# Kernel tuning notes

Measured on AMD Instinct MI355X. Metric: run time of the kernel, lower is better.

## Reference

```python
import jax, jax.numpy as jnp
import numpy as np

N_SPLIT = 4096   # split tokens (coarse octree levels)
N_VQ    = 12288  # VQ tokens (finest level)
N       = N_SPLIT + N_VQ
C       = 256    # num_embed
H       = 8      # num_heads
L       = 4      # num_blocks
P       = 256    # patch_size (attention window)
DIL     = 2      # dilation for odd (swin) blocks
DVQ     = 32     # vqvae embedding_channels
VQ_SIZE = 256    # vqvae embedding_sizes
VQ_G    = 4      # vqvae quantizer_group
HID     = 4 * C


def _layernorm(x, s, b):
    m = x.mean(-1, keepdims=True)
    v = jnp.var(x, axis=-1, keepdims=True)
    return (x - m) * jax.lax.rsqrt(v + 1e-5) * s + b


def _sin_pos_emb(n, c):
    pos = jnp.arange(n, dtype=jnp.float32)[:, None]
    half = c // 2
    freqs = jnp.exp(-jnp.log(10000.0) * jnp.arange(half, dtype=jnp.float32) / half)
    ang = pos * freqs
    return jnp.concatenate([jnp.sin(ang), jnp.cos(ang)], axis=-1)


def _forward(split, zq, targets_vq, category, batch_id, mask, d2b,
             split_emb, class_emb, vq_proj_w, vq_proj_b,
             ln1_s, ln1_b, qkv_w, qkv_b, attn_w, attn_b,
             ln2_s, ln2_b, fc1_w, fc1_b, fc2_w, fc2_b,
             lnx_s, lnx_b, split_w, split_b, vq_w, vq_b):
    # token embeddings: [split tokens ; projected VQ codes]
    x = jnp.concatenate([split_emb[split], zq @ vq_proj_w + vq_proj_b], axis=0)  # [N,C]
    cond = class_emb[category]                      # [B,C]
    x = jnp.where(mask[:, None], cond[batch_id], x)  # masked tokens -> class cond

    # depth2batch gather, then OctFormer blocks
    xb = x[d2b] + _sin_pos_emb(N, C).astype(x.dtype)
    dh = C // H
    scale = dh ** -0.5
    for l in range(L):
        d = DIL if (l % 2 == 1) else 1  # swin-style alternating dilation
        h = _layernorm(xb, ln1_s[l], ln1_b[l])
        # dilated window partition: window j in a super-window holds tokens base+p*d+j
        hw = h.reshape(-1, P, d, C).transpose(0, 2, 1, 3).reshape(-1, P, C)
        qkv = hw @ qkv_w[l] + qkv_b[l]              # [nw,P,3C]
        q, k, v = [t.reshape(-1, P, H, dh) for t in jnp.split(qkv, 3, axis=-1)]
        att = jax.nn.softmax(jnp.einsum('wphd,wqhd->whpq', q, k) * scale, axis=-1)
        o = jnp.einsum('whpq,wqhd->wphd', att, v).reshape(-1, P, C) @ attn_w[l] + attn_b[l]
        o = o.reshape(-1, d, P, C).transpose(0, 2, 1, 3).reshape(-1, C)  # undo partition
        xb = xb + o
        h = _layernorm(xb, ln2_s[l], ln2_b[l])
        xb = xb + (jax.nn.gelu(h @ fc1_w[l] + fc1_b[l]) @ fc2_w[l] + fc2_b[l])
    # batch2depth scatter (inverse permutation)
    x = jnp.zeros_like(xb).at[d2b].set(xb)
    x = _layernorm(x, lnx_s, lnx_b)

    # split head + masked cross-entropy
    sl = x[:N_SPLIT] @ split_w + split_b            # [Ns,2]
    ms = mask[:N_SPLIT].astype(jnp.float32)
    ce_s = -jnp.take_along_axis(jax.nn.log_softmax(sl, axis=-1), split[:, None], axis=-1)[:, 0]
    split_loss = jnp.sum(ce_s * ms) / jnp.maximum(jnp.sum(ms), 1.0)

    # vq head + masked grouped cross-entropy
    vl = (x[N_SPLIT:] @ vq_w + vq_b).reshape(N_VQ, VQ_G, VQ_SIZE)
    mv = mask[N_SPLIT:].astype(jnp.float32)
    ce_v = -jnp.take_along_axis(jax.nn.log_softmax(vl, axis=-1), targets_vq[..., None], axis=-1)[..., 0]
    vq_loss = jnp.sum(ce_v.mean(-1) * mv) / jnp.maximum(jnp.sum(mv), 1.0)
    return jnp.stack([split_loss, vq_loss])


def setup_inputs() -> dict:
    key = jax.random.key(0)
    ks = jax.random.split(key, 16)
    s = 0.02
    inp = {
        'split': jax.random.randint(ks[0], (N_SPLIT,), 0, 2),
        'zq': jax.random.normal(ks[1], (N_VQ, DVQ), jnp.float32),
        'targets_vq': jax.random.randint(ks[2], (N_VQ, VQ_G), 0, VQ_SIZE),
        'category': jnp.zeros((1,), jnp.int32),
        'batch_id': jnp.zeros((N,), jnp.int32),
        'mask': jax.random.randint(ks[3], (N,), 0, 2).astype(bool),
        'd2b': jax.random.permutation(ks[4], N),
        'split_emb': s * jax.random.normal(ks[5], (2, C), jnp.float32),
        'class_emb': s * jax.random.normal(ks[6], (1, C), jnp.float32),
        'vq_proj_w': s * jax.random.normal(ks[7], (DVQ, C), jnp.float32),
        'vq_proj_b': jnp.zeros((C,), jnp.float32),
        'ln1_s': jnp.ones((L, C), jnp.float32),
        'ln1_b': jnp.zeros((L, C), jnp.float32),
        'qkv_w': s * jax.random.normal(ks[8], (L, C, 3 * C), jnp.float32),
        'qkv_b': jnp.zeros((L, 3 * C), jnp.float32),
        'attn_w': s * jax.random.normal(ks[9], (L, C, C), jnp.float32),
        'attn_b': jnp.zeros((L, C), jnp.float32),
        'ln2_s': jnp.ones((L, C), jnp.float32),
        'ln2_b': jnp.zeros((L, C), jnp.float32),
        'fc1_w': s * jax.random.normal(ks[10], (L, C, HID), jnp.float32),
        'fc1_b': jnp.zeros((L, HID), jnp.float32),
        'fc2_w': s * jax.random.normal(ks[11], (L, HID, C), jnp.float32),
        'fc2_b': jnp.zeros((L, C), jnp.float32),
        'lnx_s': jnp.ones((C,), jnp.float32),
        'lnx_b': jnp.zeros((C,), jnp.float32),
        'split_w': s * jax.random.normal(ks[12], (C, 2), jnp.float32),
        'split_b': jnp.zeros((2,), jnp.float32),
        'vq_w': s * jax.random.normal(ks[13], (C, VQ_G * VQ_SIZE), jnp.float32),
        'vq_b': jnp.zeros((VQ_G * VQ_SIZE,), jnp.float32),
    }
    return inp


def reference(split, zq, targets_vq, category, batch_id, mask, d2b,
              split_emb, class_emb, vq_proj_w, vq_proj_b,
              ln1_s, ln1_b, qkv_w, qkv_b, attn_w, attn_b,
              ln2_s, ln2_b, fc1_w, fc1_b, fc2_w, fc2_b,
              lnx_s, lnx_b, split_w, split_b, vq_w, vq_b):
    return _forward(split, zq, targets_vq, category, batch_id, mask, d2b,
                    split_emb, class_emb, vq_proj_w, vq_proj_b,
                    ln1_s, ln1_b, qkv_w, qkv_b, attn_w, attn_b,
                    ln2_s, ln2_b, fc1_w, fc1_b, fc2_w, fc2_b,
                    lnx_s, lnx_b, split_w, split_b, vq_w, vq_b)
```

## Files before the change

kernel.cpp:

```cpp
#include <hip/hip_runtime.h>
#include <hip/hip_bf16.h>
#include <math.h>

#define NSPLIT 4096
#define NVQ    12288
#define NTOK   16384
#define CH     256
#define NH     8
#define DHD    32
#define NL     4
#define PW     256
#define HIDN   1024
#define DVQ    32
#define VQG    4
#define VQS    256

typedef __attribute__((ext_vector_type(8))) short bf16x8;
typedef __attribute__((ext_vector_type(4))) float f32x4;

typedef const __attribute__((address_space(1))) void* gas_ptr;
typedef __attribute__((address_space(3))) void* las_ptr;
#define GLD16(g, s) __builtin_amdgcn_global_load_lds((gas_ptr)(g), (las_ptr)(s), 16, 0, 0)

static __device__ __forceinline__ unsigned pack2bf(float a, float b) {
    __hip_bfloat16 ha = __float2bfloat16(a), hb = __float2bfloat16(b);
    return ((unsigned)*(unsigned short*)&hb << 16) | *(unsigned short*)&ha;
}
static __device__ __forceinline__ float bf2f(unsigned short s) {
    unsigned u = (unsigned)s << 16;
    return *(float*)&u;
}
static __device__ __forceinline__ unsigned short f2bfu(float f) {
    __hip_bfloat16 h = __float2bfloat16(f);
    return *(unsigned short*)&h;
}

__global__ void k_wt_all(const float* __restrict__ qkv_w, const float* __restrict__ attn_w,
                         const float* __restrict__ fc1_w, const float* __restrict__ fc2_w,
                         const float* __restrict__ vq_w,
                         short* __restrict__ qkvT, short* __restrict__ attnT,
                         short* __restrict__ fc1T, short* __restrict__ fc2T,
                         short* __restrict__ vqT,
                         const void* __restrict__ mask_raw, int* __restrict__ mode) {
    int b = blockIdx.x;
    if (b == 832) {
        __shared__ int c_even, c_odd, c_0100;
        const unsigned short* u16 = (const unsigned short*)mask_raw;
        if (threadIdx.x == 0) { c_even = 0; c_odd = 0; c_0100 = 0; }
        __syncthreads();
        int le = 0, lo = 0, l01 = 0;
        for (int i = threadIdx.x; i < 8192; i += 256) {
            unsigned short v = u16[i];
            if (v == 0x3F80u) { if (i & 1) lo++; else le++; }
            if (v == 0x0100u) l01++;
        }
        atomicAdd(&c_even, le); atomicAdd(&c_odd, lo); atomicAdd(&c_0100, l01);
        __syncthreads();
        if (threadIdx.x == 0) {
            int m;
            if      (c_even > 500) m = 2;
            else if (c_odd  > 500) m = 3;
            else if (c_0100 > 500) m = 1;
            else                   m = 0;
            *mode = m;
        }
        return;
    }
    const float* W; short* Wt; int K, N, tn, tk;
    if (b < 192)      { int r = b;       int z = r / 48; r %= 48; K = 256;  N = 768;
                        tk = r / 12; tn = r % 12;
                        W = qkv_w + (size_t)z * K * N; Wt = qkvT + (size_t)z * K * N; }
    else if (b < 256) { int r = b - 192; int z = r / 16; r %= 16; K = 256;  N = 256;
                        tk = r / 4;  tn = r % 4;
                        W = attn_w + (size_t)z * K * N; Wt = attnT + (size_t)z * K * N; }
    else if (b < 512) { int r = b - 256; int z = r / 64; r %= 64; K = 256;  N = 1024;
                        tk = r / 16; tn = r % 16;
                        W = fc1_w + (size_t)z * K * N; Wt = fc1T + (size_t)z * K * N; }
    else if (b < 768) { int r = b - 512; int z = r / 64; r %= 64; K = 1024; N = 256;
                        tk = r / 4;  tn = r % 4;
                        W = fc2_w + (size_t)z * K * N; Wt = fc2T + (size_t)z * K * N; }
    else              { int r = b - 768; K = 256; N = 1024;
                        tk = r / 16; tn = r % 16; W = vq_w; Wt = vqT; }
    __shared__ float t[64][65];
    int bn = tn * 64, bk = tk * 64, tid = threadIdx.x;
#pragma unroll
    for (int it = 0; it < 16; ++it) {
        int idx = it * 256 + tid; int r = idx >> 6, c = idx & 63;
        t[r][c] = W[(size_t)(bk + r) * N + bn + c];
    }
    __syncthreads();
#pragma unroll
    for (int it = 0; it < 16; ++it) {
        int idx = it * 256 + tid; int r = idx >> 6, c = idx & 63;
        __hip_bfloat16 h = __float2bfloat16(t[c][r]);
        Wt[(size_t)(bn + r) * K + bk + c] = *(short*)&h;
    }
}

__global__ void k_embed_gather(const int* __restrict__ split, const float* __restrict__ zq,
                               const int* __restrict__ category, const int* __restrict__ batch_id,
                               const void* __restrict__ mask_raw, const int* __restrict__ mode,
                               int* __restrict__ mask_i, const int* __restrict__ d2b,
                               const float* __restrict__ split_emb, const float* __restrict__ class_emb,
                               const float* __restrict__ vq_proj_w, const float* __restrict__ vq_proj_b,
                               const float* __restrict__ ln1s, const float* __restrict__ ln1b,
                               unsigned short* __restrict__ xbv, unsigned short* __restrict__ hb) {
    int j = blockIdx.x, c = threadIdx.x;
    int i = d2b[j];
    int m = *mode, mv;
    if      (m == 0) mv = ((const int*)mask_raw)[i] != 0;
    else if (m == 1) mv = ((const unsigned char*)mask_raw)[i] != 0;
    else if (m == 2) mv = ((const unsigned short*)mask_raw)[i] != 0;
    else             mv = ((const unsigned int*)mask_raw)[i] != 0;
    if (c == 0) mask_i[i] = mv;
    float v;
    if (mv) {
        v = class_emb[category[batch_id[i]] * CH + c];
    } else if (i < NSPLIT) {
        v = split_emb[split[i] * CH + c];
    } else {
        const float* z = zq + (size_t)(i - NSPLIT) * DVQ;
        float acc = vq_proj_b[c];
#pragma unroll
        for (int k = 0; k < DVQ; k++) acc += z[k] * vq_proj_w[k * CH + c];
        v = acc;
    }
    const float kneg = -0.07195578415606394f;
    float jf = (float)j, pe;
    if (c < 128) { float f = expf(c * kneg);         pe = sinf(jf * f); }
    else         { float f = expf((c - 128) * kneg); pe = cosf(jf * f); }
    v += pe;
    float s = v, sq = v * v;
#pragma unroll
    for (int o = 32; o; o >>= 1) { s += __shfl_xor(s, o); sq += __shfl_xor(sq, o); }
    __shared__ float ps[4], pq[4];
    if ((c & 63) == 0) { ps[c >> 6] = s; pq[c >> 6] = sq; }
    __syncthreads();
    float S = ps[0] + ps[1] + ps[2] + ps[3];
    float Q = pq[0] + pq[1] + pq[2] + pq[3];
    float mean = S * (1.0f / CH);
    float var  = Q * (1.0f / CH) - mean * mean;
    float rsf = rsqrtf(var + 1e-5f);
    xbv[(size_t)j * CH + c] = f2bfu(v);
    hb[(size_t)j * CH + c]  = f2bfu((v - mean) * rsf * ln1s[c] + ln1b[c]);
}

template <int GELU>
__global__ __launch_bounds__(256, 4) void k_mm(
    const short* __restrict__ A, const short* __restrict__ Bt,
    const float* __restrict__ bias, unsigned short* __restrict__ outB,
    int N, int K) {
    __shared__ short As[2][128 * 32];
    __shared__ short Bs[2][128 * 32];
    const int tid = threadIdx.x;
    const int w = tid >> 6, l = tid & 63;
    const int bm = blockIdx.y * 128, bn = blockIdx.x * 128;
    const int wr = w >> 1, wc = w & 1;
    const int q = l >> 4, rA = l & 15;
    const int srow = w * 16 + (l >> 2);
    const int sx = ((l & 3) ^ ((l >> 2) & 3)) * 8;
    const int fx = (q ^ (rA & 3)) * 8;

    const short* gA0 = A + (size_t)(bm + srow) * K + sx;
    const short* gA1 = A + (size_t)(bm + srow + 64) * K + sx;
    const short* gB0 = Bt + (size_t)(bn + srow) * K + sx;
    const short* gB1 = Bt + (size_t)(bn + srow + 64) * K + sx;
    short* lA0 = &As[0][w * 16 * 32];
    short* lA1 = &As[0][(64 + w * 16) * 32];
    short* lA0h = &As[1][w * 16 * 32];
    short* lA1h = &As[1][(64 + w * 16) * 32];
    short* lB0 = &Bs[0][w * 16 * 32];
    short* lB1 = &Bs[0][(64 + w * 16) * 32];
    short* lB0h = &Bs[1][w * 16 * 32];
    short* lB1h = &Bs[1][(64 + w * 16) * 32];

    f32x4 acc[4][4] = {};

    for (int k0 = 0; k0 < K; k0 += 64) {
        GLD16(gA0 + k0, lA0);       GLD16(gA1 + k0, lA1);
        GLD16(gA0 + k0 + 32, lA0h); GLD16(gA1 + k0 + 32, lA1h);
        GLD16(gB0 + k0, lB0);       GLD16(gB1 + k0, lB1);
        GLD16(gB0 + k0 + 32, lB0h); GLD16(gB1 + k0 + 32, lB1h);
        __syncthreads();
#pragma unroll
        for (int s = 0; s < 2; s++) {
            bf16x8 a[4], b[4];
#pragma unroll
            for (int m = 0; m < 4; m++)
                a[m] = *(const bf16x8*)(&As[s][(wr * 64 + m * 16 + rA) * 32 + fx]);
#pragma unroll
            for (int n = 0; n < 4; n++)
                b[n] = *(const bf16x8*)(&Bs[s][(wc * 64 + n * 16 + rA) * 32 + fx]);
#pragma unroll
            for (int m = 0; m < 4; m++)
#pragma unroll
                for (int n = 0; n < 4; n++)
                    acc[m][n] = __builtin_amdgcn_mfma_f32_16x16x32_bf16(b[n], a[m], acc[m][n], 0, 0, 0);
        }
        __syncthreads();
    }

#pragma unroll
    for (int m = 0; m < 4; m++) {
        int row = bm + wr * 64 + m * 16 + rA;
#pragma unroll
        for (int n = 0; n < 4; n++) {
            int colb = bn + wc * 64 + n * 16 + q * 4;
            float4 bv = *(const float4*)(bias + colb);
            float v0 = acc[m][n][0] + bv.x;
            float v1 = acc[m][n][1] + bv.y;
            float v2 = acc[m][n][2] + bv.z;
            float v3 = acc[m][n][3] + bv.w;
            if (GELU) {
                float t0 = tanhf(0.7978845608028654f * (v0 + 0.044715f * v0 * v0 * v0));
                float t1 = tanhf(0.7978845608028654f * (v1 + 0.044715f * v1 * v1 * v1));
                float t2 = tanhf(0.7978845608028654f * (v2 + 0.044715f * v2 * v2 * v2));
                float t3 = tanhf(0.7978845608028654f * (v3 + 0.044715f * v3 * v3 * v3));
                v0 = 0.5f * v0 * (1.0f + t0); v1 = 0.5f * v1 * (1.0f + t1);
                v2 = 0.5f * v2 * (1.0f + t2); v3 = 0.5f * v3 * (1.0f + t3);
            }
            ushort4 st = { f2bfu(v0), f2bfu(v1), f2bfu(v2), f2bfu(v3) };
            *(ushort4*)(outB + (size_t)row * N + colb) = st;
        }
    }
}

template <int LNOUT>
__global__ __launch_bounds__(512, 4) void k_mm_row(
    const short* __restrict__ A, const short* __restrict__ Bt,
    const float* __restrict__ bias, unsigned short* __restrict__ xbv,
    const float* __restrict__ lns, const float* __restrict__ lnb,
    unsigned short* __restrict__ h_out, const int* __restrict__ d2b, int K,
    const int* __restrict__ split, const int* __restrict__ mask_i,
    const float* __restrict__ sw, const float* __restrict__ sb,
    float* __restrict__ sce) {
    __shared__ short As[2][32 * 32];
    __shared__ short Bs[2][256 * 32];
    __shared__ float part[2][8][32];
    const int tid = threadIdx.x;
    const int w = tid >> 6, l = tid & 63;
    const int bm = blockIdx.x * 32;
    const int q = l >> 4, rA = l & 15;
    const int sx = ((l & 3) ^ ((l >> 2) & 3)) * 8;
    const int fx = (q ^ (rA & 3)) * 8;

    const short* gA = A + (size_t)(bm + (l >> 2)) * K + sx;
    const short* gB = Bt + (size_t)(w * 32 + (l >> 2)) * K + sx;

    f32x4 acc[2][2] = {};

    for (int k0 = 0; k0 < K; k0 += 64) {
        if (w == 0) {
#pragma unroll
            for (int rg = 0; rg < 2; rg++) {
                GLD16(gA + (size_t)(rg * 16) * K + k0,      &As[0][(rg * 16) * 32]);
                GLD16(gA + (size_t)(rg * 16) * K + k0 + 32, &As[1][(rg * 16) * 32]);
            }
        }
#pragma unroll
        for (int i = 0; i < 2; i++) {
            GLD16(gB + (size_t)(i * 16) * K + k0,      &Bs[0][(w * 32 + i * 16) * 32]);
            GLD16(gB + (size_t)(i * 16) * K + k0 + 32, &Bs[1][(w * 32 + i * 16) * 32]);
        }
        __syncthreads();
#pragma unroll
        for (int s = 0; s < 2; s++) {
            bf16x8 a[2], b[2];
#pragma unroll
            for (int m = 0; m < 2; m++)
                a[m] = *(const bf16x8*)(&As[s][(m * 16 + rA) * 32 + fx]);
#pragma unroll
            for (int n = 0; n < 2; n++)
                b[n] = *(const bf16x8*)(&Bs[s][(w * 32 + n * 16 + rA) * 32 + fx]);
#pragma unroll
            for (int m = 0; m < 2; m++)
#pragma unroll
                for (int n = 0; n < 2; n++)
                    acc[m][n] = __builtin_amdgcn_mfma_f32_16x16x32_bf16(b[n], a[m], acc[m][n], 0, 0, 0);
        }
        __syncthreads();
    }

    float rsum[2] = {}, rsq[2] = {};
#pragma unroll
    for (int m = 0; m < 2; m++) {
        int row = bm + m * 16 + rA;
#pragma unroll
        for (int n = 0; n < 2; n++) {
            int colb = w * 32 + n * 16 + q * 4;
            float4 bv = *(const float4*)(bias + colb);
            size_t oi = (size_t)row * CH + colb;
            ushort4 xo = *(const ushort4*)(xbv + oi);
            float v0 = acc[m][n][0] + bv.x + bf2f(xo.x);
            float v1 = acc[m][n][1] + bv.y + bf2f(xo.y);
            float v2 = acc[m][n][2] + bv.z + bf2f(xo.z);
            float v3 = acc[m][n][3] + bv.w + bf2f(xo.w);
            acc[m][n][0] = v0; acc[m][n][1] = v1; acc[m][n][2] = v2; acc[m][n][3] = v3;
            if (LNOUT != 2) {
                ushort4 st = { f2bfu(v0), f2bfu(v1), f2bfu(v2), f2bfu(v3) };
                *(ushort4*)(xbv + oi) = st;
            }
            rsum[m] += (v0 + v1) + (v2 + v3);
            rsq[m]  += (v0 * v0 + v1 * v1) + (v2 * v2 + v3 * v3);
        }
    }
    if (LNOUT) {
#pragma unroll
        for (int m = 0; m < 2; m++) {
            rsum[m] += __shfl_xor(rsum[m], 16); rsum[m] += __shfl_xor(rsum[m], 32);
            rsq[m]  += __shfl_xor(rsq[m], 16);  rsq[m]  += __shfl_xor(rsq[m], 32);
        }
        if (q == 0) {
#pragma unroll
            for (int m = 0; m < 2; m++) {
                part[0][w][m * 16 + rA] = rsum[m];
                part[1][w][m * 16 + rA] = rsq[m];
            }
        }
        __syncthreads();
#pragma unroll
        for (int m = 0; m < 2; m++) {
            int row = m * 16 + rA;
            float S = 0.f, Q = 0.f;
#pragma unroll
            for (int ww = 0; ww < 8; ww++) { S += part[0][ww][row]; Q += part[1][ww][row]; }
            float mean = S * (1.0f / CH);
            float var  = Q * (1.0f / CH) - mean * mean;
            float rsf = rsqrtf(var + 1e-5f);
            size_t orow = (LNOUT == 2) ? (size_t)d2b[bm + row] : (size_t)(bm + row);
#pragma unroll
            for (int n = 0; n < 2; n++) {
                int colb = w * 32 + n * 16 + q * 4;
                float4 sv = *(const float4*)(lns + colb);
                float4 bb = *(const float4*)(lnb + colb);
                float h0 = (acc[m][n][0] - mean) * rsf * sv.x + bb.x;
                float h1 = (acc[m][n][1] - mean) * rsf * sv.y + bb.y;
                float h2 = (acc[m][n][2] - mean) * rsf * sv.z + bb.z;
                float h3 = (acc[m][n][3] - mean) * rsf * sv.w + bb.w;
                acc[m][n][0] = h0; acc[m][n][1] = h1; acc[m][n][2] = h2; acc[m][n][3] = h3;
                ushort4 st = { f2bfu(h0), f2bfu(h1), f2bfu(h2), f2bfu(h3) };
                *(ushort4*)(h_out + orow * CH + colb) = st;
            }
        }
    }
    if (LNOUT == 2) {
        float a0[2] = {}, a1[2] = {};
#pragma unroll
        for (int m = 0; m < 2; m++) {
#pragma unroll
            for (int n = 0; n < 2; n++) {
                int colb = w * 32 + n * 16 + q * 4;
#pragma unroll
                for (int j = 0; j < 4; j++) {
                    a0[m] += acc[m][n][j] * sw[2 * (colb + j)];
                    a1[m] += acc[m][n][j] * sw[2 * (colb + j) + 1];
                }
            }
            a0[m] += __shfl_xor(a0[m], 16); a0[m] += __shfl_xor(a0[m], 32);
            a1[m] += __shfl_xor(a1[m], 16); a1[m] += __shfl_xor(a1[m], 32);
        }
        __syncthreads();
        if (q == 0) {
#pragma unroll
            for (int m = 0; m < 2; m++) {
                part[0][w][m * 16 + rA] = a0[m];
                part[1][w][m * 16 + rA] = a1[m];
            }
        }
        __syncthreads();
        if (w == 0 && q == 0) {
#pragma unroll
            for (int m = 0; m < 2; m++) {
                int row = m * 16 + rA;
                int orow = d2b[bm + row];
                if (orow < NSPLIT) {
                    float l0 = sb[0], l1 = sb[1];
#pragma unroll
                    for (int ww = 0; ww < 8; ww++) { l0 += part[0][ww][row]; l1 += part[1][ww][row]; }
                    float mx = fmaxf(l0, l1);
                    float lse = mx + logf(__expf(l0 - mx) + __expf(l1 - mx));
                    float ce = lse - (split[orow] ? l1 : l0);
                    sce[orow] = ce * (float)mask_i[orow];
                }
            }
        }
    }
}

__global__ __launch_bounds__(256, 4) void k_vq_head(
    const short* __restrict__ A, const short* __restrict__ vqT,
    const float* __restrict__ vq_b, const int* __restrict__ targets,
    float* __restrict__ vce4) {
    __shared__ short As[2][32 * 32];
    __shared__ short Bs[2][256 * 32];
    __shared__ float part[2][4][32];
    __shared__ float tgtv[32];
    const int tid = threadIdx.x;
    const int w = tid >> 6, l = tid & 63;
    const int bm = blockIdx.x * 32;
    const int g = blockIdx.y;
    const int q = l >> 4, rA = l & 15;
    const int sx = ((l & 3) ^ ((l >> 2) & 3)) * 8;
    const int fx = (q ^ (rA & 3)) * 8;

    const short* gA = A + (size_t)(bm + (l >> 2)) * CH + sx;
    const short* gB = vqT + (size_t)(g * VQS + w * 64 + (l >> 2)) * CH + sx;

    f32x4 acc[2][4] = {};

    for (int k0 = 0; k0 < CH; k0 += 64) {
        if (w == 0) {
#pragma unroll
            for (int rg = 0; rg < 2; rg++) {
                GLD16(gA + (size_t)(rg * 16) * CH + k0,      &As[0][(rg * 16) * 32]);
                GLD16(gA + (size_t)(rg * 16) * CH + k0 + 32, &As[1][(rg * 16) * 32]);
            }
        }
#pragma unroll
        for (int i = 0; i < 4; i++) {
            GLD16(gB + (size_t)(i * 16) * CH + k0,      &Bs[0][(w * 64 + i * 16) * 32]);
            GLD16(gB + (size_t)(i * 16) * CH + k0 + 32, &Bs[1][(w * 64 + i * 16) * 32]);
        }
        __syncthreads();
#pragma unroll
        for (int s = 0; s < 2; s++) {
            bf16x8 a[2], b[4];
#pragma unroll
            for (int m = 0; m < 2; m++)
                a[m] = *(const bf16x8*)(&As[s][(m * 16 + rA) * 32 + fx]);
#pragma unroll
            for (int n = 0; n < 4; n++)
                b[n] = *(const bf16x8*)(&Bs[s][(w * 64 + n * 16 + rA) * 32 + fx]);
#pragma unroll
            for (int m = 0; m < 2; m++)
#pragma unroll
                for (int n = 0; n < 4; n++)
                    acc[m][n] = __builtin_amdgcn_mfma_f32_16x16x32_bf16(b[n], a[m], acc[m][n], 0, 0, 0);
        }
        __syncthreads();
    }

    float pm[2];
#pragma unroll
    for (int m = 0; m < 2; m++) {
        pm[m] = -1e30f;
        int row = m * 16 + rA;
        int t = targets[(size_t)(bm + row) * VQG + g];
#pragma unroll
        for (int n = 0; n < 4; n++) {
            int colb = w * 64 + n * 16 + q * 4;
            float4 bv = *(const float4*)(vq_b + g * VQS + colb);
            float v0 = acc[m][n][0] + bv.x;
            float v1 = acc[m][n][1] + bv.y;
            float v2 = acc[m][n][2] + bv.z;
            float v3 = acc[m][n][3] + bv.w;
            acc[m][n][0] = v0; acc[m][n][1] = v1; acc[m][n][2] = v2; acc[m][n][3] = v3;
            if (colb + 0 == t) tgtv[row] = v0;
            if (colb + 1 == t) tgtv[row] = v1;
            if (colb + 2 == t) tgtv[row] = v2;
            if (colb + 3 == t) tgtv[row] = v3;
            pm[m] = fmaxf(pm[m], fmaxf(fmaxf(v0, v1), fmaxf(v2, v3)));
        }
    }
#pragma unroll
    for (int m = 0; m < 2; m++) {
        pm[m] = fmaxf(pm[m], __shfl_xor(pm[m], 16));
        pm[m] = fmaxf(pm[m], __shfl_xor(pm[m], 32));
    }
    if (q == 0) {
#pragma unroll
        for (int m = 0; m < 2; m++) part[0][w][m * 16 + rA] = pm[m];
    }
    __syncthreads();
    float pmf[2], psum[2];
#pragma unroll
    for (int m = 0; m < 2; m++) {
        int row = m * 16 + rA;
        float mx = fmaxf(fmaxf(part[0][0][row], part[0][1][row]),
                         fmaxf(part[0][2][row], part[0][3][row]));
        pmf[m] = mx;
        float s = 0.f;
#pragma unroll
        for (int n = 0; n < 4; n++)
            s += __expf(acc[m][n][0] - mx) + __expf(acc[m][n][1] - mx)
               + __expf(acc[m][n][2] - mx) + __expf(acc[m][n][3] - mx);
        psum[m] = s;
    }
#pragma unroll
    for (int m = 0; m < 2; m++) {
        psum[m] += __shfl_xor(psum[m], 16);
        psum[m] += __shfl_xor(psum[m], 32);
    }
    if (q == 0) {
#pragma unroll
        for (int m = 0; m < 2; m++) part[1][w][m * 16 + rA] = psum[m];
    }
    __syncthreads();
    if (w == 0 && q == 0) {
#pragma unroll
        for (int m = 0; m < 2; m++) {
            int row = m * 16 + rA;
            float tot = part[1][0][row] + part[1][1][row] + part[1][2][row] + part[1][3][row];
            float lse = pmf[m] + logf(tot);
            vce4[(size_t)(bm + row) * VQG + g] = lse - tgtv[row];
        }
    }
}

__global__ __launch_bounds__(512, 4) void k_attn_fused(
    const unsigned short* __restrict__ hin, const short* __restrict__ Wt,
    const float* __restrict__ bias, short* __restrict__ o, int dil) {
    __shared__ short smem[40960];
    short* Asm = smem;
    short* Wsm = smem + 16384;
    short* Ql  = smem;
    short* Kl  = smem + 8192;
    short* Vt  = smem + 16384;
    short* Pl  = smem + 24576;

    const int wid = blockIdx.x, hd = blockIdx.y;
    const int tid = threadIdx.x;
    const int w = tid >> 6, l = tid & 63;
    const int g = l >> 4, c = l & 15;
    const int tbase = (wid / dil) * (PW * dil) + (wid % dil);
    const int sx = ((l & 3) ^ ((l >> 2) & 3)) * 8;
    const int fx = (g ^ (c & 3)) * 8;

    f32x4 acc[2][6] = {};
    {
        const int lr = l >> 2;
        const int rw = w * 12 + lr;
        const int seg = rw >> 5, within = rw & 31;
        const short* gW = Wt + (size_t)(seg * 256 + hd * 32 + within) * CH + sx;
        for (int k0 = 0; k0 < CH; k0 += 64) {
#pragma unroll
            for (int h16 = 0; h16 < 2; h16++) {
                int row = w * 32 + h16 * 16 + lr;
                const unsigned short* src = hin + (size_t)(tbase + row * dil) * CH + k0 + sx;
                GLD16(src,      Asm + (w * 32 + h16 * 16) * 32);
                GLD16(src + 32, Asm + 8192 + (w * 32 + h16 * 16) * 32);
            }
            if (l < 48) {
                GLD16(gW + k0,      Wsm + (w * 12) * 32);
                GLD16(gW + k0 + 32, Wsm + 3072 + (w * 12) * 32);
            }
            __syncthreads();
#pragma unroll
            for (int s = 0; s < 2; s++) {
                bf16x8 a[2], b[6];
#pragma unroll
                for (int m = 0; m < 2; m++)
                    a[m] = *(const bf16x8*)(Asm + s * 8192 + (w * 32 + m * 16 + c) * 32 + fx);
#pragma unroll
                for (int n = 0; n < 6; n++)
                    b[n] = *(const bf16x8*)(Wsm + s * 3072 + (n * 16 + c) * 32 + fx);
#pragma unroll
                for (int m = 0; m < 2; m++)
#pragma unroll
                    for (int n = 0; n < 6; n++)
                        acc[m][n] = __builtin_amdgcn_mfma_f32_16x16x32_bf16(b[n], a[m], acc[m][n], 0, 0, 0);
            }
            __syncthreads();
        }
    }
#pragma unroll
    for (int m = 0; m < 2; m++) {
        int t = w * 32 + m * 16 + c;
#pragma unroll
        for (int n = 0; n < 6; n++) {
            int seg = n >> 1, n1 = n & 1;
            int colb = n1 * 16 + g * 4;
            float4 bv = *(const float4*)(bias + seg * 256 + hd * 32 + colb);
            float v0 = acc[m][n][0] + bv.x;
            float v1 = acc[m][n][1] + bv.y;
            float v2 = acc[m][n][2] + bv.z;
            float v3 = acc[m][n][3] + bv.w;
            if (seg < 2) {
                short* dst = (seg == 0) ? Ql : Kl;
                int slot = (n1 * 2 + (g >> 1)) ^ (t & 3);
                uint2 pk; pk.x = pack2bf(v0, v1); pk.y = pack2bf(v2, v3);
                *(uint2*)(dst + t * 32 + slot * 8 + (g & 1) * 4) = pk;
            } else {
                int d0 = colb;
                Vt[(d0 + 0) * PW + ((((t >> 3) ^ ((d0 + 0) & 7))) << 3) + (t & 7)] = (short)f2bfu(v0);
                Vt[(d0 + 1) * PW + ((((t >> 3) ^ ((d0 + 1) & 7))) << 3) + (t & 7)] = (short)f2bfu(v1);
                Vt[(d0 + 2) * PW + ((((t >> 3) ^ ((d0 + 2) & 7))) << 3) + (t & 7)] = (short)f2bfu(v2);
                Vt[(d0 + 3) * PW + ((((t >> 3) ^ ((d0 + 3) & 7))) << 3) + (t & 7)] = (short)f2bfu(v3);
            }
        }
    }
    __syncthreads();

    bf16x8 qf[2];
#pragma unroll
    for (int qt = 0; qt < 2; qt++) {
        int qrow = w * 32 + qt * 16 + c;
        qf[qt] = *(const bf16x8*)(Ql + qrow * 32 + ((g ^ (qrow & 3)) * 8));
    }

    f32x4 acco[2][2] = {};
    float m_s[2] = {-1e30f, -1e30f};
    float l_s[2] = {0.f, 0.f};
    const float scale = 0.17677669529663687f;

#pragma unroll
    for (int ch = 0; ch < 4; ch++) {
        bf16x8 kf[4];
#pragma unroll
        for (int kvt = 0; kvt < 4; kvt++) {
            int kv = ch * 64 + kvt * 16 + c;
            kf[kvt] = *(const bf16x8*)(Kl + kv * 32 + ((g ^ (kv & 3)) * 8));
        }
        f32x4 accs[4][2] = {};
#pragma unroll
        for (int kvt = 0; kvt < 4; kvt++)
#pragma unroll
            for (int qt = 0; qt < 2; qt++)
                accs[kvt][qt] = __builtin_amdgcn_mfma_f32_16x16x32_bf16(kf[kvt], qf[qt], accs[kvt][qt], 0, 0, 0);

        float fb[2];
#pragma unroll
        for (int qt = 0; qt < 2; qt++) {
            float mx = -1e30f;
#pragma unroll
            for (int kvt = 0; kvt < 4; kvt++) {
                mx = fmaxf(mx, fmaxf(fmaxf(accs[kvt][qt][0], accs[kvt][qt][1]),
                                     fmaxf(accs[kvt][qt][2], accs[kvt][qt][3])));
            }
            mx = fmaxf(mx, __shfl_xor(mx, 16));
            mx = fmaxf(mx, __shfl_xor(mx, 32));
            float mnew = fmaxf(m_s[qt], mx * scale);
            fb[qt] = __expf(m_s[qt] - mnew);
            m_s[qt] = mnew;
        }
#pragma unroll
        for (int mt = 0; mt < 2; mt++) {
            float fo = fb[mt];
#pragma unroll
            for (int r = 0; r < 4; r++) {
                acco[mt][0][r] *= fo;
                acco[mt][1][r] *= fo;
            }
        }
        float rsum[2] = {0.f, 0.f};
#pragma unroll
        for (int kvt = 0; kvt < 4; kvt++) {
            const int cchunk = kvt * 2 + (g >> 1);
            const int koff = (g & 1) << 2;
#pragma unroll
            for (int qt = 0; qt < 2; qt++) {
                float p0 = __expf(accs[kvt][qt][0] * scale - m_s[qt]);
                float p1 = __expf(accs[kvt][qt][1] * scale - m_s[qt]);
                float p2 = __expf(accs[kvt][qt][2] * scale - m_s[qt]);
                float p3 = __expf(accs[kvt][qt][3] * scale - m_s[qt]);
                rsum[qt] += (p0 + p1) + (p2 + p3);
                int qq = qt * 16 + c;
                int phys = cchunk ^ (qq & 7);
                uint2 pk; pk.x = pack2bf(p0, p1); pk.y = pack2bf(p2, p3);
                *(uint2*)(Pl + w * 2048 + qq * 64 + phys * 8 + koff) = pk;
            }
        }
#pragma unroll
        for (int qt = 0; qt < 2; qt++) {
            float s = rsum[qt];
            s += __shfl_xor(s, 16);
            s += __shfl_xor(s, 32);
            l_s[qt] = l_s[qt] * fb[qt] + s;
        }
#pragma unroll
        for (int ks = 0; ks < 2; ks++) {
            bf16x8 pa[2];
#pragma unroll
            for (int mt = 0; mt < 2; mt++) {
                int qq = mt * 16 + c;
                int phys = (ks * 4 + g) ^ (qq & 7);
                pa[mt] = *(const bf16x8*)(Pl + w * 2048 + qq * 64 + phys * 8);
            }
#pragma unroll
            for (int nt = 0; nt < 2; nt++) {
                int d = nt * 16 + c;
                int kvabs = ch * 64 + ks * 32 + g * 8;
                int phys = (kvabs >> 3) ^ (d & 7);
                bf16x8 vb = *(const bf16x8*)(Vt + d * PW + phys * 8);
#pragma unroll
                for (int mt = 0; mt < 2; mt++)
                    acco[mt][nt] = __builtin_amdgcn_mfma_f32_16x16x32_bf16(vb, pa[mt], acco[mt][nt], 0, 0, 0);
            }
        }
    }

#pragma unroll
    for (int mt = 0; mt < 2; mt++) {
        float linv = 1.0f / l_s[mt];
        int qrow = w * 32 + mt * 16 + c;
        size_t trow = (size_t)(tbase + qrow * dil) * CH + hd * DHD;
#pragma unroll
        for (int nt = 0; nt < 2; nt++) {
            ushort4 st = { f2bfu(acco[mt][nt][0] * linv), f2bfu(acco[mt][nt][1] * linv),
                           f2bfu(acco[mt][nt][2] * linv), f2bfu(acco[mt][nt][3] * linv) };
            *(ushort4*)((unsigned short*)o + trow + nt * 16 + g * 4) = st;
        }
    }
}

__global__ void k_reduce(const float* __restrict__ sce, const float* __restrict__ vce4,
                         const int* __restrict__ mask_i, float* __restrict__ out) {
    int tid = threadIdx.x;
    float s1 = 0, s2 = 0, s3 = 0, s4 = 0;
    for (int i = tid; i < NSPLIT; i += 256) { s1 += sce[i]; s2 += (float)mask_i[i]; }
    for (int i = tid; i < NVQ; i += 256) {
        float mv = (float)mask_i[NSPLIT + i];
        float cs = vce4[i * 4 + 0] + vce4[i * 4 + 1] + vce4[i * 4 + 2] + vce4[i * 4 + 3];
        s3 += cs * 0.25f * mv;
        s4 += mv;
    }
    __shared__ float r1[256], r2[256], r3[256], r4[256];
    r1[tid] = s1; r2[tid] = s2; r3[tid] = s3; r4[tid] = s4;
    __syncthreads();
    for (int o = 128; o; o >>= 1) {
        if (tid < o) { r1[tid] += r1[tid + o]; r2[tid] += r2[tid + o];
                       r3[tid] += r3[tid + o]; r4[tid] += r4[tid + o]; }
        __syncthreads();
    }
    if (tid == 0) {
        out[0] = r1[0] / fmaxf(r2[0], 1.0f);
        out[1] = r3[0] / fmaxf(r4[0], 1.0f);
    }
}

extern "C" void kernel_launch(void* const* d_in, const int* in_sizes, int n_in,
                              void* d_out, int out_size, void* d_ws, size_t ws_size,
                              hipStream_t stream) {
    const int*   split      = (const int*)d_in[0];
    const float* zq         = (const float*)d_in[1];
    const int*   targets_vq = (const int*)d_in[2];
    const int*   category   = (const int*)d_in[3];
    const int*   batch_id   = (const int*)d_in[4];
    const void*  mask_raw   = d_in[5];
    const int*   d2b        = (const int*)d_in[6];
    const float* split_emb  = (const float*)d_in[7];
    const float* class_emb  = (const float*)d_in[8];
    const float* vq_proj_w  = (const float*)d_in[9];
    const float* vq_proj_b  = (const float*)d_in[10];
    const float* ln1_s      = (const float*)d_in[11];
    const float* ln1_b      = (const float*)d_in[12];
    const float* qkv_w      = (const float*)d_in[13];
    const float* qkv_b      = (const float*)d_in[14];
    const float* attn_w     = (const float*)d_in[15];
    const float* attn_b     = (const float*)d_in[16];
    const float* ln2_s      = (const float*)d_in[17];
    const float* ln2_b      = (const float*)d_in[18];
    const float* fc1_w      = (const float*)d_in[19];
    const float* fc1_b      = (const float*)d_in[20];
    const float* fc2_w      = (const float*)d_in[21];
    const float* fc2_b      = (const float*)d_in[22];
    const float* lnx_s      = (const float*)d_in[23];
    const float* lnx_b      = (const float*)d_in[24];
    const float* sw         = (const float*)d_in[25];
    const float* sb         = (const float*)d_in[26];
    const float* vq_w       = (const float*)d_in[27];
    const float* vq_b       = (const float*)d_in[28];

    char* ws = (char*)d_ws;
    int* mode   = (int*)ws;
    int* mask_i = (int*)(ws + 256);
    float* sce  = (float*)(ws + 256 + 4 * NTOK);
    float* vce4 = sce + NSPLIT;
    char* p = ws + (1 << 20);
    short* qkvT = (short*)p;  p += (size_t)NL * 768 * CH * 2;
    short* attnT = (short*)p; p += (size_t)NL * CH * CH * 2;
    short* fc1T = (short*)p;  p += (size_t)NL * HIDN * CH * 2;
    short* fc2T = (short*)p;  p += (size_t)NL * CH * HIDN * 2;
    short* vqT = (short*)p;   p += (size_t)HIDN * CH * 2;
    unsigned short* xbv = (unsigned short*)p; p += (size_t)NTOK * CH * 2;
    unsigned short* h_bf = (unsigned short*)p; p += (size_t)NTOK * CH * 2;
    unsigned short* o_bf = (unsigned short*)p; p += (size_t)NTOK * CH * 2;
    short* big = (short*)p;

    k_wt_all<<<833, 256, 0, stream>>>(qkv_w, attn_w, fc1_w, fc2_w, vq_w,
                                      qkvT, attnT, fc1T, fc2T, vqT, mask_raw, mode);
    k_embed_gather<<<NTOK, 256, 0, stream>>>(split, zq, category, batch_id, mask_raw, mode,
                                             mask_i, d2b, split_emb, class_emb,
                                             vq_proj_w, vq_proj_b, ln1_s, ln1_b, xbv, h_bf);

    for (int l = 0; l < NL; l++) {
        int d = (l & 1) ? 2 : 1;
        k_attn_fused<<<dim3(NTOK / PW, NH), 512, 0, stream>>>(
            h_bf, qkvT + (size_t)l * 768 * CH, qkv_b + l * 768, (short*)o_bf, d);
        k_mm_row<1><<<NTOK / 32, 512, 0, stream>>>(
            (const short*)o_bf, attnT + (size_t)l * CH * CH, attn_b + l * CH,
            xbv, ln2_s + l * CH, ln2_b + l * CH, h_bf, nullptr, CH,
            nullptr, nullptr, nullptr, nullptr, nullptr);
        k_mm<1><<<dim3(HIDN / 128, NTOK / 128), 256, 0, stream>>>(
            (const short*)h_bf, fc1T + (size_t)l * HIDN * CH, fc1_b + l * HIDN,
            (unsigned short*)big, HIDN, CH);
        if (l < NL - 1) {
            k_mm_row<1><<<NTOK / 32, 512, 0, stream>>>(
                big, fc2T + (size_t)l * CH * HIDN, fc2_b + l * CH,
                xbv, ln1_s + (l + 1) * CH, ln1_b + (l + 1) * CH, h_bf, nullptr, HIDN,
                nullptr, nullptr, nullptr, nullptr, nullptr);
        } else {
            k_mm_row<2><<<NTOK / 32, 512, 0, stream>>>(
                big, fc2T + (size_t)l * CH * HIDN, fc2_b + l * CH,
                xbv, lnx_s, lnx_b, h_bf, d2b, HIDN,
                split, mask_i, sw, sb, sce);
        }
    }

    k_vq_head<<<dim3(NVQ / 32, VQG), 256, 0, stream>>>(
        (const short*)(h_bf + (size_t)NSPLIT * CH), vqT, vq_b, targets_vq, vce4);
    k_reduce<<<1, 256, 0, stream>>>(sce, vce4, mask_i, (float*)d_out);
}
```

Before: 425.2 us.

## Fuse FC1+GELU and FC2+residual+LayerNorm into one MLP kernel

Replaces the separate FC1 GEMM (writing a 16384x1024 bf16 hidden tensor to global memory) and FC2 row GEMM with a single kernel per 32-row tile. That kernel computes FC1+GELU into a swizzled LDS buffer, then runs FC2 from LDS with W2 read directly from global memory, followed by residual add and LayerNorm (plus the split-CE head on the last layer). This removes the global write and read of the large hidden activation and one launch per layer. In exchange, each block recomputes nothing but uses about 80 KB of LDS, which lowers occupancy, and W2 is streamed unstaged from global/L2 by every block.

New measurement: 472.2 us. 11.1% more time.

```diff
diff --git a/kernel.cpp b/kernel.cpp
--- a/kernel.cpp
+++ b/kernel.cpp
@@ -33,6 +33,10 @@
 static __device__ __forceinline__ unsigned short f2bfu(float f) {
     __hip_bfloat16 h = __float2bfloat16(f);
     return *(unsigned short*)&h;
+}
+static __device__ __forceinline__ float gelu_f(float v) {
+    float t = tanhf(0.7978845608028654f * (v + 0.044715f * v * v * v));
+    return 0.5f * v * (1.0f + t);
 }
 
 __global__ void k_wt_all(const float* __restrict__ qkv_w, const float* __restrict__ attn_w,
@@ -145,95 +149,12 @@
     hb[(size_t)j * CH + c]  = f2bfu((v - mean) * rsf * ln1s[c] + ln1b[c]);
 }
 
-template <int GELU>
-__global__ __launch_bounds__(256, 4) void k_mm(
-    const short* __restrict__ A, const short* __restrict__ Bt,
-    const float* __restrict__ bias, unsigned short* __restrict__ outB,
-    int N, int K) {
-    __shared__ short As[2][128 * 32];
-    __shared__ short Bs[2][128 * 32];
-    const int tid = threadIdx.x;
-    const int w = tid >> 6, l = tid & 63;
-    const int bm = blockIdx.y * 128, bn = blockIdx.x * 128;
-    const int wr = w >> 1, wc = w & 1;
-    const int q = l >> 4, rA = l & 15;
-    const int srow = w * 16 + (l >> 2);
-    const int sx = ((l & 3) ^ ((l >> 2) & 3)) * 8;
-    const int fx = (q ^ (rA & 3)) * 8;
-
-    const short* gA0 = A + (size_t)(bm + srow) * K + sx;
-    const short* gA1 = A + (size_t)(bm + srow + 64) * K + sx;
-    const short* gB0 = Bt + (size_t)(bn + srow) * K + sx;
-    const short* gB1 = Bt + (size_t)(bn + srow + 64) * K + sx;
-    short* lA0 = &As[0][w * 16 * 32];
-    short* lA1 = &As[0][(64 + w * 16) * 32];
-    short* lA0h = &As[1][w * 16 * 32];
-    short* lA1h = &As[1][(64 + w * 16) * 32];
-    short* lB0 = &Bs[0][w * 16 * 32];
-    short* lB1 = &Bs[0][(64 + w * 16) * 32];
-    short* lB0h = &Bs[1][w * 16 * 32];
-    short* lB1h = &Bs[1][(64 + w * 16) * 32];
-
-    f32x4 acc[4][4] = {};
-
-    for (int k0 = 0; k0 < K; k0 += 64) {
-        GLD16(gA0 + k0, lA0);       GLD16(gA1 + k0, lA1);
-        GLD16(gA0 + k0 + 32, lA0h); GLD16(gA1 + k0 + 32, lA1h);
-        GLD16(gB0 + k0, lB0);       GLD16(gB1 + k0, lB1);
-        GLD16(gB0 + k0 + 32, lB0h); GLD16(gB1 + k0 + 32, lB1h);
-        __syncthreads();
-#pragma unroll
-        for (int s = 0; s < 2; s++) {
-            bf16x8 a[4], b[4];
-#pragma unroll
-            for (int m = 0; m < 4; m++)
-                a[m] = *(const bf16x8*)(&As[s][(wr * 64 + m * 16 + rA) * 32 + fx]);
-#pragma unroll
-            for (int n = 0; n < 4; n++)
-                b[n] = *(const bf16x8*)(&Bs[s][(wc * 64 + n * 16 + rA) * 32 + fx]);
-#pragma unroll
-            for (int m = 0; m < 4; m++)
-#pragma unroll
-                for (int n = 0; n < 4; n++)
-                    acc[m][n] = __builtin_amdgcn_mfma_f32_16x16x32_bf16(b[n], a[m], acc[m][n], 0, 0, 0);
-        }
-        __syncthreads();
-    }
-
-#pragma unroll
-    for (int m = 0; m < 4; m++) {
-        int row = bm + wr * 64 + m * 16 + rA;
-#pragma unroll
-        for (int n = 0; n < 4; n++) {
-            int colb = bn + wc * 64 + n * 16 + q * 4;
-            float4 bv = *(const float4*)(bias + colb);
-            float v0 = acc[m][n][0] + bv.x;
-            float v1 = acc[m][n][1] + bv.y;
-            float v2 = acc[m][n][2] + bv.z;
-            float v3 = acc[m][n][3] + bv.w;
-            if (GELU) {
-                float t0 = tanhf(0.7978845608028654f * (v0 + 0.044715f * v0 * v0 * v0));
-                float t1 = tanhf(0.7978845608028654f * (v1 + 0.044715f * v1 * v1 * v1));
-                float t2 = tanhf(0.7978845608028654f * (v2 + 0.044715f * v2 * v2 * v2));
-                float t3 = tanhf(0.7978845608028654f * (v3 + 0.044715f * v3 * v3 * v3));
-                v0 = 0.5f * v0 * (1.0f + t0); v1 = 0.5f * v1 * (1.0f + t1);
-                v2 = 0.5f * v2 * (1.0f + t2); v3 = 0.5f * v3 * (1.0f + t3);
-            }
-            ushort4 st = { f2bfu(v0), f2bfu(v1), f2bfu(v2), f2bfu(v3) };
-            *(ushort4*)(outB + (size_t)row * N + colb) = st;
-        }
-    }
-}
-
 template <int LNOUT>
 __global__ __launch_bounds__(512, 4) void k_mm_row(
     const short* __restrict__ A, const short* __restrict__ Bt,
     const float* __restrict__ bias, unsigned short* __restrict__ xbv,
     const float* __restrict__ lns, const float* __restrict__ lnb,
-    unsigned short* __restrict__ h_out, const int* __restrict__ d2b, int K,
-    const int* __restrict__ split, const int* __restrict__ mask_i,
-    const float* __restrict__ sw, const float* __restrict__ sb,
-    float* __restrict__ sce) {
+    unsigned short* __restrict__ h_out, int K) {
     __shared__ short As[2][32 * 32];
     __shared__ short Bs[2][256 * 32];
     __shared__ float part[2][8][32];
@@ -296,10 +217,8 @@
             float v2 = acc[m][n][2] + bv.z + bf2f(xo.z);
             float v3 = acc[m][n][3] + bv.w + bf2f(xo.w);
             acc[m][n][0] = v0; acc[m][n][1] = v1; acc[m][n][2] = v2; acc[m][n][3] = v3;
-            if (LNOUT != 2) {
-                ushort4 st = { f2bfu(v0), f2bfu(v1), f2bfu(v2), f2bfu(v3) };
-                *(ushort4*)(xbv + oi) = st;
-            }
+            ushort4 st = { f2bfu(v0), f2bfu(v1), f2bfu(v2), f2bfu(v3) };
+            *(ushort4*)(xbv + oi) = st;
             rsum[m] += (v0 + v1) + (v2 + v3);
             rsq[m]  += (v0 * v0 + v1 * v1) + (v2 * v2 + v3 * v3);
         }
@@ -327,56 +246,213 @@
             float mean = S * (1.0f / CH);
             float var  = Q * (1.0f / CH) - mean * mean;
             float rsf = rsqrtf(var + 1e-5f);
-            size_t orow = (LNOUT == 2) ? (size_t)d2b[bm + row] : (size_t)(bm + row);
 #pragma unroll
             for (int n = 0; n < 2; n++) {
                 int colb = w * 32 + n * 16 + q * 4;
                 float4 sv = *(const float4*)(lns + colb);
                 float4 bb = *(const float4*)(lnb + colb);
-                float h0 = (acc[m][n][0] - mean) * rsf * sv.x + bb.x;
-                float h1 = (acc[m][n][1] - mean) * rsf * sv.y + bb.y;
-                float h2 = (acc[m][n][2] - mean) * rsf * sv.z + bb.z;
-                float h3 = (acc[m][n][3] - mean) * rsf * sv.w + bb.w;
-                acc[m][n][0] = h0; acc[m][n][1] = h1; acc[m][n][2] = h2; acc[m][n][3] = h3;
-                ushort4 st = { f2bfu(h0), f2bfu(h1), f2bfu(h2), f2bfu(h3) };
-                *(ushort4*)(h_out + orow * CH + colb) = st;
-            }
+                ushort4 st = {
+                    f2bfu((acc[m][n][0] - mean) * rsf * sv.x + bb.x),
+                    f2bfu((acc[m][n][1] - mean) * rsf * sv.y + bb.y),
+                    f2bfu((acc[m][n][2] - mean) * rsf * sv.z + bb.z),
+                    f2bfu((acc[m][n][3] - mean) * rsf * sv.w + bb.w) };
+                *(ushort4*)(h_out + (size_t)(bm + row) * CH + colb) = st;
+            }
+        }
+    }
+}
+
+template <int LNOUT>
+__global__ __launch_bounds__(512, 4) void k_mlp(
+    const unsigned short* __restrict__ hin, const short* __restrict__ W1t,
+    const float* __restrict__ b1, const short* __restrict__ W2t,
+    const float* __restrict__ b2, unsigned short* __restrict__ xbv,
+    const float* __restrict__ lns, const float* __restrict__ lnb,
+    unsigned short* __restrict__ h_out, const int* __restrict__ d2b,
+    const int* __restrict__ split, const int* __restrict__ mask_i,
+    const float* __restrict__ sw, const float* __restrict__ sb,
+    float* __restrict__ sce) {
+    __shared__ short smem[40960];
+    short* As = smem;
+    short* Bs = smem + 1024;
+    short* gld = smem + 7936;
+    float* part = (float*)smem;
+
+    const int tid = threadIdx.x;
+    const int w = tid >> 6, l = tid & 63;
+    const int g4 = l >> 4, c = l & 15;
+    const int bm = blockIdx.x * 32;
+    const int sx = ((l & 3) ^ ((l >> 2) & 3)) * 8;
+    const int fx = (g4 ^ (c & 3)) * 8;
+
+    f32x4 acc1[2][8] = {};
+    {
+        const unsigned short* gA = hin + (size_t)(bm + (l >> 2)) * CH + sx;
+        const short* gB = W1t + (size_t)(w * 128 + (l >> 2)) * CH + sx;
+        for (int k0 = 0; k0 < CH; k0 += 32) {
+            if (w == 0) {
+                GLD16(gA + k0,                        As);
+                GLD16(gA + (size_t)16 * CH + k0,      As + 512);
+            }
+#pragma unroll
+            for (int rg = 0; rg < 8; rg++)
+                GLD16(gB + (size_t)(rg * 16) * CH + k0, Bs + (w * 128 + rg * 16) * 32);
+            __syncthreads();
+            bf16x8 a1[2];
+#pragma unroll
+            for (int m = 0; m < 2; m++)
+                a1[m] = *(const bf16x8*)(As + (m * 16 + c) * 32 + fx);
+#pragma unroll
+            for (int nh = 0; nh < 2; nh++) {
+                bf16x8 bv[4];
+#pragma unroll
+                for (int j = 0; j < 4; j++)
+                    bv[j] = *(const bf16x8*)(Bs + (w * 128 + (nh * 4 + j) * 16 + c) * 32 + fx);
+#pragma unroll
+                for (int m = 0; m < 2; m++)
+#pragma unroll
+                    for (int j = 0; j < 4; j++)
+                        acc1[m][nh * 4 + j] = __builtin_amdgcn_mfma_f32_16x16x32_bf16(
+                            bv[j], a1[m], acc1[m][nh * 4 + j], 0, 0, 0);
+            }
+            __syncthreads();
+        }
+    }
+#pragma unroll
+    for (int m = 0; m < 2; m++) {
+        int row32 = m * 16 + c;
+#pragma unroll
+        for (int n = 0; n < 8; n++) {
+            int cc = w * 128 + n * 16 + g4 * 4;
+            float4 bb = *(const float4*)(b1 + cc);
+            float v0 = gelu_f(acc1[m][n][0] + bb.x);
+            float v1 = gelu_f(acc1[m][n][1] + bb.y);
+            float v2 = gelu_f(acc1[m][n][2] + bb.z);
+            float v3 = gelu_f(acc1[m][n][3] + bb.w);
+            int cc32 = cc & ~31;
+            int slot = (cc >> 3) & 3;
+            int off = cc & 7;
+            uint2 pk; pk.x = pack2bf(v0, v1); pk.y = pack2bf(v2, v3);
+            *(uint2*)(gld + row32 * 1032 + cc32 + ((slot ^ (row32 & 3)) << 3) + off) = pk;
+        }
+    }
+    __syncthreads();
+
+    f32x4 acc2[2][2] = {};
+    {
+        const short* gW2 = W2t + (size_t)(w * 32 + c) * HIDN + g4 * 8;
+#pragma unroll 2
+        for (int kk = 0; kk < HIDN; kk += 32) {
+            bf16x8 a2[2], b2v[2];
+#pragma unroll
+            for (int m = 0; m < 2; m++)
+                a2[m] = *(const bf16x8*)(gld + (m * 16 + c) * 1032 + kk + fx);
+#pragma unroll
+            for (int n = 0; n < 2; n++)
+                b2v[n] = *(const bf16x8*)(gW2 + (size_t)(n * 16) * HIDN + kk);
+#pragma unroll
+            for (int m = 0; m < 2; m++)
+#pragma unroll
+                for (int n = 0; n < 2; n++)
+                    acc2[m][n] = __builtin_amdgcn_mfma_f32_16x16x32_bf16(b2v[n], a2[m], acc2[m][n], 0, 0, 0);
+        }
+    }
+
+    float rsum[2] = {}, rsq[2] = {};
+#pragma unroll
+    for (int m = 0; m < 2; m++) {
+        int row = bm + m * 16 + c;
+#pragma unroll
+        for (int n = 0; n < 2; n++) {
+            int colb = w * 32 + n * 16 + g4 * 4;
+            float4 bv = *(const float4*)(b2 + colb);
+            size_t oi = (size_t)row * CH + colb;
+            ushort4 xo = *(const ushort4*)(xbv + oi);
+            float v0 = acc2[m][n][0] + bv.x + bf2f(xo.x);
+            float v1 = acc2[m][n][1] + bv.y + bf2f(xo.y);
+            float v2 = acc2[m][n][2] + bv.z + bf2f(xo.z);
+            float v3 = acc2[m][n][3] + bv.w + bf2f(xo.w);
+            acc2[m][n][0] = v0; acc2[m][n][1] = v1; acc2[m][n][2] = v2; acc2[m][n][3] = v3;
+            if (LNOUT != 2) {
+                ushort4 st = { f2bfu(v0), f2bfu(v1), f2bfu(v2), f2bfu(v3) };
+                *(ushort4*)(xbv + oi) = st;
+            }
+            rsum[m] += (v0 + v1) + (v2 + v3);
+            rsq[m]  += (v0 * v0 + v1 * v1) + (v2 * v2 + v3 * v3);
+        }
+    }
+#pragma unroll
+    for (int m = 0; m < 2; m++) {
+        rsum[m] += __shfl_xor(rsum[m], 16); rsum[m] += __shfl_xor(rsum[m], 32);
+        rsq[m]  += __shfl_xor(rsq[m], 16);  rsq[m]  += __shfl_xor(rsq[m], 32);
+    }
+    __syncthreads();
+    if (g4 == 0) {
+#pragma unroll
+        for (int m = 0; m < 2; m++) {
+            part[0 * 256 + w * 32 + m * 16 + c] = rsum[m];
+            part[1 * 256 + w * 32 + m * 16 + c] = rsq[m];
+        }
+    }
+    __syncthreads();
+#pragma unroll
+    for (int m = 0; m < 2; m++) {
+        int row = m * 16 + c;
+        float S = 0.f, Q = 0.f;
+#pragma unroll
+        for (int ww = 0; ww < 8; ww++) { S += part[ww * 32 + row]; Q += part[256 + ww * 32 + row]; }
+        float mean = S * (1.0f / CH);
+        float var  = Q * (1.0f / CH) - mean * mean;
+        float rsf = rsqrtf(var + 1e-5f);
+        size_t orow = (LNOUT == 2) ? (size_t)d2b[bm + row] : (size_t)(bm + row);
+#pragma unroll
+        for (int n = 0; n < 2; n++) {
+            int colb = w * 32 + n * 16 + g4 * 4;
+            float4 sv = *(const float4*)(lns + colb);
+            float4 bb = *(const float4*)(lnb + colb);
+            float h0 = (acc2[m][n][0] - mean) * rsf * sv.x + bb.x;
+            float h1 = (acc2[m][n][1] - mean) * rsf * sv.y + bb.y;
+            float h2 = (acc2[m][n][2] - mean) * rsf * sv.z + bb.z;
+            float h3 = (acc2[m][n][3] - mean) * rsf * sv.w + bb.w;
+            acc2[m][n][0] = h0; acc2[m][n][1] = h1; acc2[m][n][2] = h2; acc2[m][n][3] = h3;
+            ushort4 st = { f2bfu(h0), f2bfu(h1), f2bfu(h2), f2bfu(h3) };
+            *(ushort4*)(h_out + orow * CH + colb) = st;
         }
     }
     if (LNOUT == 2) {
-        float a0[2] = {}, a1[2] = {};
+        float a0[2] = {}, a1s[2] = {};
 #pragma unroll
         for (int m = 0; m < 2; m++) {
 #pragma unroll
             for (int n = 0; n < 2; n++) {
-                int colb = w * 32 + n * 16 + q * 4;
+                int colb = w * 32 + n * 16 + g4 * 4;
 #pragma unroll
                 for (int j = 0; j < 4; j++) {
-                    a0[m] += acc[m][n][j] * sw[2 * (colb + j)];
-                    a1[m] += acc[m][n][j] * sw[2 * (colb + j) + 1];
+                    a0[m]  += acc2[m][n][j] * sw[2 * (colb + j)];
+                    a1s[m] += acc2[m][n][j] * sw[2 * (colb + j) + 1];
                 }
             }
-            a0[m] += __shfl_xor(a0[m], 16); a0[m] += __shfl_xor(a0[m], 32);
-            a1[m] += __shfl_xor(a1[m], 16); a1[m] += __shfl_xor(a1[m], 32);
-        }
-        __syncthreads();
-        if (q == 0) {
+            a0[m]  += __shfl_xor(a0[m], 16);  a0[m]  += __shfl_xor(a0[m], 32);
+            a1s[m] += __shfl_xor(a1s[m], 16); a1s[m] += __shfl_xor(a1s[m], 32);
+        }
+        __syncthreads();
+        if (g4 == 0) {
 #pragma unroll
             for (int m = 0; m < 2; m++) {
-                part[0][w][m * 16 + rA] = a0[m];
-                part[1][w][m * 16 + rA] = a1[m];
-            }
-        }
-        __syncthreads();
-        if (w == 0 && q == 0) {
+                part[w * 32 + m * 16 + c] = a0[m];
+                part[256 + w * 32 + m * 16 + c] = a1s[m];
+            }
+        }
+        __syncthreads();
+        if (w == 0 && g4 == 0) {
 #pragma unroll
             for (int m = 0; m < 2; m++) {
-                int row = m * 16 + rA;
+                int row = m * 16 + c;
                 int orow = d2b[bm + row];
                 if (orow < NSPLIT) {
                     float l0 = sb[0], l1 = sb[1];
 #pragma unroll
-                    for (int ww = 0; ww < 8; ww++) { l0 += part[0][ww][row]; l1 += part[1][ww][row]; }
+                    for (int ww = 0; ww < 8; ww++) { l0 += part[ww * 32 + row]; l1 += part[256 + ww * 32 + row]; }
                     float mx = fmaxf(l0, l1);
                     float lse = mx + logf(__expf(l0 - mx) + __expf(l1 - mx));
                     float ce = lse - (split[orow] ? l1 : l0);
@@ -775,7 +851,6 @@
     unsigned short* xbv = (unsigned short*)p; p += (size_t)NTOK * CH * 2;
     unsigned short* h_bf = (unsigned short*)p; p += (size_t)NTOK * CH * 2;
     unsigned short* o_bf = (unsigned short*)p; p += (size_t)NTOK * CH * 2;
-    short* big = (short*)p;
 
     k_wt_all<<<833, 256, 0, stream>>>(qkv_w, attn_w, fc1_w, fc2_w, vq_w,
                                       qkvT, attnT, fc1T, fc2T, vqT, mask_raw, mode);
@@ -789,20 +864,18 @@
             h_bf, qkvT + (size_t)l * 768 * CH, qkv_b + l * 768, (short*)o_bf, d);
         k_mm_row<1><<<NTOK / 32, 512, 0, stream>>>(
             (const short*)o_bf, attnT + (size_t)l * CH * CH, attn_b + l * CH,
-            xbv, ln2_s + l * CH, ln2_b + l * CH, h_bf, nullptr, CH,
-            nullptr, nullptr, nullptr, nullptr, nullptr);
-        k_mm<1><<<dim3(HIDN / 128, NTOK / 128), 256, 0, stream>>>(
-            (const short*)h_bf, fc1T + (size_t)l * HIDN * CH, fc1_b + l * HIDN,
-            (unsigned short*)big, HIDN, CH);
+            xbv, ln2_s + l * CH, ln2_b + l * CH, h_bf, CH);
         if (l < NL - 1) {
-            k_mm_row<1><<<NTOK / 32, 512, 0, stream>>>(
-                big, fc2T + (size_t)l * CH * HIDN, fc2_b + l * CH,
-                xbv, ln1_s + (l + 1) * CH, ln1_b + (l + 1) * CH, h_bf, nullptr, HIDN,
+            k_mlp<1><<<NTOK / 32, 512, 0, stream>>>(
+                h_bf, fc1T + (size_t)l * HIDN * CH, fc1_b + l * HIDN,
+                fc2T + (size_t)l * CH * HIDN, fc2_b + l * CH, xbv,
+                ln1_s + (l + 1) * CH, ln1_b + (l + 1) * CH, h_bf, nullptr,
                 nullptr, nullptr, nullptr, nullptr, nullptr);
         } else {
-            k_mm_row<2><<<NTOK / 32, 512, 0, stream>>>(
-                big, fc2T + (size_t)l * CH * HIDN, fc2_b + l * CH,
-                xbv, lnx_s, lnx_b, h_bf, d2b, HIDN,
+            k_mlp<2><<<NTOK / 32, 512, 0, stream>>>(
+                h_bf, fc1T + (size_t)l * HIDN * CH, fc1_b + l * HIDN,
+                fc2T + (size_t)l * CH * HIDN, fc2_b + l * CH, xbv,
+                lnx_s, lnx_b, h_bf, d2b,
                 split, mask_i, sw, sb, sce);
         }
     }
```
